# Optimization experiments

Measured on AMD Instinct MI355X. Metric: run time of the kernel, lower is better.

The kernel has to match this reference:

```python
import jax, jax.numpy as jnp
import numpy as np

VOCAB = 32
UTT_LEN = 16
NUM_MEANING_TYPES = 5
MEANINGS_PER_TYPE = 10
SUPPORT_SIZE = 100000  # = MEANINGS_PER_TYPE ** NUM_MEANING_TYPES
BATCH = 2048


def setup_inputs() -> dict:
    key = jax.random.key(0)
    k1, k2, k3 = jax.random.split(key, 3)
    # query utterances: [utt_len, batch] token ids
    utts = jax.random.randint(k1, (UTT_LEN, BATCH), 0, VOCAB, dtype=jnp.int64)
    # support set is stored as one-hot encoded utterances [S, utt_len*vocab]
    support_tokens = jax.random.randint(k2, (SUPPORT_SIZE, UTT_LEN), 0, VOCAB)
    support = jax.nn.one_hot(support_tokens, VOCAB, dtype=jnp.float32)
    support = support.reshape(SUPPORT_SIZE, UTT_LEN * VOCAB)
    # meanings table [S, num_meaning_types]
    meanings_t = jax.random.randint(k3, (SUPPORT_SIZE, NUM_MEANING_TYPES), 0,
                                    MEANINGS_PER_TYPE, dtype=jnp.int64)
    return {"utts": utts, "support": support, "meanings_t": meanings_t}


def reference(utts, support, meanings_t):
    # utts: [M, N] ints; support: [S, M*V] floats; meanings_t: [S, T] ints
    M, N = utts.shape
    # one-hot encode queries: [N, M, V] -> [N, M*V]
    batch_fluffy = jax.nn.one_hot(utts.T, VOCAB, dtype=jnp.float32).reshape(N, M * VOCAB)
    batch_sq = jnp.sum(batch_fluffy * batch_fluffy, axis=1)        # [N]
    support_sq = jnp.sum(support * support, axis=1)                # [S]
    cross = batch_fluffy @ support.T                                # [N, S]
    squared_dist = batch_sq[:, None] + support_sq[None, :] - 2.0 * cross
    # top-1 smallest distance (K=1)
    top1 = jnp.argmin(squared_dist, axis=1)                         # [N]
    meanings = meanings_t[top1]                                     # [N, T]
    return jax.nn.one_hot(meanings, MEANINGS_PER_TYPE, dtype=jnp.float32)
```

## Files before the change

kernel.cpp:

```cpp
#include <hip/hip_runtime.h>
#include <stdint.h>

#define S_ROWS 100000
#define NQ     2048
#define M_POS  16
#define VOCABS 32
#define WPB    8
#define GROUPS 8
#define CHUNKS 125
#define RC     800
#define KITER  25
#define KPAD   264

__global__ __launch_bounds__(256) void knn_decode(const float* __restrict__ support,
                                                  uint8_t* __restrict__ tok,
                                                  uint32_t* __restrict__ best) {
    if (blockIdx.x < 8) best[blockIdx.x * 256 + threadIdx.x] = 0u;
    int wave = (blockIdx.x * 256 + threadIdx.x) >> 6;
    int lane = threadIdx.x & 63;
    if (wave >= S_ROWS) return;
    const float4* rowp = (const float4*)(support + (size_t)wave * 512) + lane * 2;
    float4 f0 = rowp[0];
    float4 f1 = rowp[1];
    float base = (float)((lane & 3) * 64);
    float v = f0.x * (base + 0.f)  + f0.y * (base + 8.f)  + f0.z * (base + 16.f) + f0.w * (base + 24.f)
            + f1.x * (base + 32.f) + f1.y * (base + 40.f) + f1.z * (base + 48.f) + f1.w * (base + 56.f);
    v += __shfl_xor(v, 1);
    v += __shfl_xor(v, 2);
    if ((lane & 3) == 0) {
        int p = lane >> 2;
        tok[(size_t)wave * 16 + p] = (uint8_t)(v + 0.5f);
    }
}

__device__ __forceinline__ void FA(uint32_t a, uint32_t b, uint32_t c,
                                   uint32_t& s, uint32_t& co) {
    uint32_t x = a ^ b;
    s  = x ^ c;
    co = (a & b) | (x & c);
}
__device__ __forceinline__ void HA(uint32_t a, uint32_t b, uint32_t& s, uint32_t& co) {
    s = a ^ b; co = a & b;
}

__device__ __forceinline__ void gather16(const uint32_t* __restrict__ tw, uint4 ta,
                                         uint32_t b[16]) {
    b[0]  = tw[ (ta.x        & 0xFFu) +  0*256];
    b[1]  = tw[((ta.x >> 8)  & 0xFFu) +  1*256];
    b[2]  = tw[((ta.x >> 16) & 0xFFu) +  2*256];
    b[3]  = tw[((ta.x >> 24)        ) +  3*256];
    b[4]  = tw[ (ta.y        & 0xFFu) +  4*256];
    b[5]  = tw[((ta.y >> 8)  & 0xFFu) +  5*256];
    b[6]  = tw[((ta.y >> 16) & 0xFFu) +  6*256];
    b[7]  = tw[((ta.y >> 24)        ) +  7*256];
    b[8]  = tw[ (ta.z        & 0xFFu) +  8*256];
    b[9]  = tw[((ta.z >> 8)  & 0xFFu) +  9*256];
    b[10] = tw[((ta.z >> 16) & 0xFFu) + 10*256];
    b[11] = tw[((ta.z >> 24)        ) + 11*256];
    b[12] = tw[ (ta.w        & 0xFFu) + 12*256];
    b[13] = tw[((ta.w >> 8)  & 0xFFu) + 13*256];
    b[14] = tw[((ta.w >> 16) & 0xFFu) + 14*256];
    b[15] = tw[((ta.w >> 24)        ) + 15*256];
}

__device__ __forceinline__ void score_row(const uint32_t b[16], int k,
        uint32_t& cp0, uint32_t& cp1, uint32_t& cp2, uint32_t& cp3, uint32_t& cp4,
        uint32_t& k0p, uint32_t& k1p, uint32_t& k2p, uint32_t& k3p, uint32_t& k4p) {
    uint32_t s10,s11,s12,s13,s14, c10,c11,c12,c13,c14;
    FA(b[0],b[1],b[2],   s10,c10);
    FA(b[3],b[4],b[5],   s11,c11);
    FA(b[6],b[7],b[8],   s12,c12);
    FA(b[9],b[10],b[11], s13,c13);
    FA(b[12],b[13],b[14],s14,c14);
    uint32_t s2a,c2a,s2b,c2b;
    FA(s10,s11,s12, s2a,c2a);
    FA(s13,s14,b[15], s2b,c2b);
    uint32_t n0,h0;  HA(s2a,s2b, n0,h0);
    uint32_t u,cu,vv,cv,x2,cx,n1,cy;
    FA(c10,c11,c12, u,cu);
    FA(c13,c14,c2a, vv,cv);
    FA(u,vv,c2b,    x2,cx);
    HA(x2,h0,       n1,cy);
    uint32_t y4,cz,n2,cw,n3,n4;
    FA(cu,cv,cx, y4,cz);
    HA(y4,cy,    n2,cw);
    HA(cz,cw,    n3,n4);

    uint32_t eq = ~(n4 ^ cp4);
    uint32_t gt = n4 & ~cp4;
    gt |= eq & (n3 & ~cp3);  eq &= ~(n3 ^ cp3);
    gt |= eq & (n2 & ~cp2);  eq &= ~(n2 ^ cp2);
    gt |= eq & (n1 & ~cp1);  eq &= ~(n1 ^ cp1);
    gt |= eq & (n0 & ~cp0);

    uint32_t ng = ~gt;
    cp0 = (gt & n0) | (ng & cp0);
    cp1 = (gt & n1) | (ng & cp1);
    cp2 = (gt & n2) | (ng & cp2);
    cp3 = (gt & n3) | (ng & cp3);
    cp4 = (gt & n4) | (ng & cp4);
    uint32_t kb0 = 0u - (uint32_t)( k       & 1);
    uint32_t kb1 = 0u - (uint32_t)((k >> 1) & 1);
    uint32_t kb2 = 0u - (uint32_t)((k >> 2) & 1);
    uint32_t kb3 = 0u - (uint32_t)((k >> 3) & 1);
    uint32_t kb4 = 0u - (uint32_t)((k >> 4) & 1);
    k0p = (k0p & ng) | (gt & kb0);
    k1p = (k1p & ng) | (gt & kb1);
    k2p = (k2p & ng) | (gt & kb2);
    k3p = (k3p & ng) | (gt & kb3);
    k4p = (k4p & ng) | (gt & kb4);
}

__global__ __launch_bounds__(256, 4)
__attribute__((amdgpu_waves_per_eu(4, 4)))
void knn_score(const int* __restrict__ utts,
               const uint8_t* __restrict__ tok,
               uint32_t* __restrict__ best) {
    __shared__ uint32_t smem[32 * KPAD];
    uint32_t* table = smem;
    uint32_t* keys  = smem;

    const int bid = blockIdx.x;
    const int g   = bid & 7;
    const int c   = bid >> 3;
    const int t   = threadIdx.x;

    #pragma unroll
    for (int i = 0; i < 16; ++i) table[t + 256 * i] = 0u;
    __syncthreads();

    {
        int q = g * 256 + t;
        int wb = t >> 5, j = t & 31;
        #pragma unroll
        for (int m = 0; m < M_POS; ++m) {
            int v = utts[m * NQ + q];
            atomicOr(&table[(m * VOCABS + v) * WPB + wb], 1u << j);
        }
    }
    __syncthreads();

    const int w   = t & 7;
    const int sub = t >> 3;
    const int r0  = c * RC;
    const uint32_t* tw = table + w;

    uint32_t cp0=0,cp1=0,cp2=0,cp3=0,cp4=0;
    uint32_t k0p=0,k1p=0,k2p=0,k3p=0,k4p=0;

    const uint4* tbase = (const uint4*)(tok + (size_t)(r0 + sub) * 16);

    uint4 tA = tbase[0];
    uint4 tB = tbase[32];
    #pragma unroll 1
    for (int j = 0; j < 12; ++j) {
        uint4 tAn, tBn;
        if (j < 11) {
            tAn = tbase[32 * (2 * j + 2)];
            tBn = tbase[32 * (2 * j + 3)];
        } else {
            tAn = tbase[32 * 24];
            tBn = tAn;
        }
        uint32_t b0[16], b1[16];
        gather16(tw, tA, b0);
        gather16(tw, tB, b1);
        score_row(b0, 2 * j,     cp0,cp1,cp2,cp3,cp4, k0p,k1p,k2p,k3p,k4p);
        score_row(b1, 2 * j + 1, cp0,cp1,cp2,cp3,cp4, k0p,k1p,k2p,k3p,k4p);
        tA = tAn; tB = tBn;
    }
    {
        uint32_t b0[16];
        gather16(tw, tA, b0);
        score_row(b0, 24, cp0,cp1,cp2,cp3,cp4, k0p,k1p,k2p,k3p,k4p);
    }

    __syncthreads();

    {
        uint32_t C = 0x1FFFFu - (uint32_t)(r0 + sub);
        #pragma unroll
        for (int j = 0; j < 32; ++j) {
            uint32_t cnt = ((cp0>>j)&1u) | (((cp1>>j)&1u)<<1) | (((cp2>>j)&1u)<<2)
                         | (((cp3>>j)&1u)<<3) | (((cp4>>j)&1u)<<4);
            uint32_t kk  = ((k0p>>j)&1u) | (((k1p>>j)&1u)<<1) | (((k2p>>j)&1u)<<2)
                         | (((k3p>>j)&1u)<<3) | (((k4p>>j)&1u)<<4);
            uint32_t key = (cnt << 17) + C - (kk << 5);
            keys[j * KPAD + t] = key;
        }
    }
    __syncthreads();

    {
        int w2 = t & 7, j2 = t >> 3;
        const uint32_t* kp = keys + j2 * KPAD + w2;
        uint32_t bestv = 0;
        #pragma unroll
        for (int i = 0; i < 32; ++i) {
            uint32_t v = kp[8 * i];
            bestv = bestv > v ? bestv : v;
        }
        atomicMax(&best[g * 256 + w2 * 32 + j2], bestv);
    }
}

__global__ __launch_bounds__(256) void knn_out(const uint32_t* __restrict__ best,
                                               const int* __restrict__ meanings,
                                               float* __restrict__ out) {
    int q = blockIdx.x * 256 + threadIdx.x;
    if (q >= NQ) return;
    uint32_t b = best[q];
    int idx = 0x1FFFF - (int)(b & 0x1FFFFu);
    float* o = out + (size_t)q * 50;
    #pragma unroll
    for (int tt = 0; tt < 5; ++tt) {
        int mv = meanings[(size_t)idx * 5 + tt];
        #pragma unroll
        for (int mm = 0; mm < 10; ++mm) o[tt * 10 + mm] = (mm == mv) ? 1.0f : 0.0f;
    }
}

extern "C" void kernel_launch(void* const* d_in, const int* in_sizes, int n_in,
                              void* d_out, int out_size, void* d_ws, size_t ws_size,
                              hipStream_t stream) {
    const int*   utts     = (const int*)d_in[0];
    const float* support  = (const float*)d_in[1];
    const int*   meanings = (const int*)d_in[2];
    float* out = (float*)d_out;

    uint8_t*  tok  = (uint8_t*)d_ws;
    uint32_t* best = (uint32_t*)((char*)d_ws + (size_t)S_ROWS * 16);

    knn_decode<<<(S_ROWS + 3) / 4, 256, 0, stream>>>(support, tok, best);
    knn_score<<<GROUPS * CHUNKS, 256, 0, stream>>>(utts, tok, best);
    knn_out<<<NQ / 256, 256, 0, stream>>>(best, meanings, out);
}
```

Baseline: 314.3 us.

## Widen query tile to 1024 per block and reduce support rows per thread

Each score block now covers 1024 queries (32 bitmask words per table entry) instead of 256, so every decoded support-row token load and the address computation behind each gather serve four times as many queries. Rows per thread-column drop to 8 with 50 rows each, which needs a sixth bit for the row index, and there are now 500 blocks of the 2×250 grid. The bitset table grows to 64KB of LDS with occupancy lowered to 2 waves per EU. Fewer waves may hide LDS gather latency less well, and the larger table may conflict more in LDS banks.

Measured after the change: 352.9 us. 12.3% more time.

```diff
diff --git a/kernel.cpp b/kernel.cpp
--- a/kernel.cpp
+++ b/kernel.cpp
@@ -5,11 +5,11 @@
 #define NQ     2048
 #define M_POS  16
 #define VOCABS 32
-#define WPB    8
-#define GROUPS 8
-#define CHUNKS 125
-#define RC     800
-#define KITER  25
+#define GROUPS 2
+#define CHUNKS 250
+#define RC     400
+#define SUBS   8
+#define NPAIR  25
 #define KPAD   264
 
 __global__ __launch_bounds__(256) void knn_decode(const float* __restrict__ support,
@@ -43,29 +43,30 @@
     s = a ^ b; co = a & b;
 }
 
-__device__ __forceinline__ void gather16(const uint32_t* __restrict__ tw, uint4 ta,
+__device__ __forceinline__ void gather16(const char* __restrict__ tb, uint4 ta,
                                          uint32_t b[16]) {
-    b[0]  = tw[ (ta.x        & 0xFFu) +  0*256];
-    b[1]  = tw[((ta.x >> 8)  & 0xFFu) +  1*256];
-    b[2]  = tw[((ta.x >> 16) & 0xFFu) +  2*256];
-    b[3]  = tw[((ta.x >> 24)        ) +  3*256];
-    b[4]  = tw[ (ta.y        & 0xFFu) +  4*256];
-    b[5]  = tw[((ta.y >> 8)  & 0xFFu) +  5*256];
-    b[6]  = tw[((ta.y >> 16) & 0xFFu) +  6*256];
-    b[7]  = tw[((ta.y >> 24)        ) +  7*256];
-    b[8]  = tw[ (ta.z        & 0xFFu) +  8*256];
-    b[9]  = tw[((ta.z >> 8)  & 0xFFu) +  9*256];
-    b[10] = tw[((ta.z >> 16) & 0xFFu) + 10*256];
-    b[11] = tw[((ta.z >> 24)        ) + 11*256];
-    b[12] = tw[ (ta.w        & 0xFFu) + 12*256];
-    b[13] = tw[((ta.w >> 8)  & 0xFFu) + 13*256];
-    b[14] = tw[((ta.w >> 16) & 0xFFu) + 14*256];
-    b[15] = tw[((ta.w >> 24)        ) + 15*256];
+    b[0]  = *(const uint32_t*)(tb + ( ta.x        & 0xFFu) * 16 +  0*4096);
+    b[1]  = *(const uint32_t*)(tb + ((ta.x >> 8)  & 0xFFu) * 16 +  1*4096);
+    b[2]  = *(const uint32_t*)(tb + ((ta.x >> 16) & 0xFFu) * 16 +  2*4096);
+    b[3]  = *(const uint32_t*)(tb + ((ta.x >> 24)        ) * 16 +  3*4096);
+    b[4]  = *(const uint32_t*)(tb + ( ta.y        & 0xFFu) * 16 +  4*4096);
+    b[5]  = *(const uint32_t*)(tb + ((ta.y >> 8)  & 0xFFu) * 16 +  5*4096);
+    b[6]  = *(const uint32_t*)(tb + ((ta.y >> 16) & 0xFFu) * 16 +  6*4096);
+    b[7]  = *(const uint32_t*)(tb + ((ta.y >> 24)        ) * 16 +  7*4096);
+    b[8]  = *(const uint32_t*)(tb + ( ta.z        & 0xFFu) * 16 +  8*4096);
+    b[9]  = *(const uint32_t*)(tb + ((ta.z >> 8)  & 0xFFu) * 16 +  9*4096);
+    b[10] = *(const uint32_t*)(tb + ((ta.z >> 16) & 0xFFu) * 16 + 10*4096);
+    b[11] = *(const uint32_t*)(tb + ((ta.z >> 24)        ) * 16 + 11*4096);
+    b[12] = *(const uint32_t*)(tb + ( ta.w        & 0xFFu) * 16 + 12*4096);
+    b[13] = *(const uint32_t*)(tb + ((ta.w >> 8)  & 0xFFu) * 16 + 13*4096);
+    b[14] = *(const uint32_t*)(tb + ((ta.w >> 16) & 0xFFu) * 16 + 14*4096);
+    b[15] = *(const uint32_t*)(tb + ((ta.w >> 24)        ) * 16 + 15*4096);
 }
 
 __device__ __forceinline__ void score_row(const uint32_t b[16], int k,
         uint32_t& cp0, uint32_t& cp1, uint32_t& cp2, uint32_t& cp3, uint32_t& cp4,
-        uint32_t& k0p, uint32_t& k1p, uint32_t& k2p, uint32_t& k3p, uint32_t& k4p) {
+        uint32_t& k0p, uint32_t& k1p, uint32_t& k2p, uint32_t& k3p, uint32_t& k4p,
+        uint32_t& k5p) {
     uint32_t s10,s11,s12,s13,s14, c10,c11,c12,c13,c14;
     FA(b[0],b[1],b[2],   s10,c10);
     FA(b[3],b[4],b[5],   s11,c11);
@@ -104,75 +105,72 @@
     uint32_t kb2 = 0u - (uint32_t)((k >> 2) & 1);
     uint32_t kb3 = 0u - (uint32_t)((k >> 3) & 1);
     uint32_t kb4 = 0u - (uint32_t)((k >> 4) & 1);
+    uint32_t kb5 = 0u - (uint32_t)((k >> 5) & 1);
     k0p = (k0p & ng) | (gt & kb0);
     k1p = (k1p & ng) | (gt & kb1);
     k2p = (k2p & ng) | (gt & kb2);
     k3p = (k3p & ng) | (gt & kb3);
     k4p = (k4p & ng) | (gt & kb4);
-}
-
-__global__ __launch_bounds__(256, 4)
-__attribute__((amdgpu_waves_per_eu(4, 4)))
+    k5p = (k5p & ng) | (gt & kb5);
+}
+
+__global__ __launch_bounds__(256)
+__attribute__((amdgpu_waves_per_eu(2, 2)))
 void knn_score(const int* __restrict__ utts,
                const uint8_t* __restrict__ tok,
                uint32_t* __restrict__ best) {
-    __shared__ uint32_t smem[32 * KPAD];
-    uint32_t* table = smem;
-    uint32_t* keys  = smem;
+    __shared__ uint32_t smem[16384];
 
     const int bid = blockIdx.x;
-    const int g   = bid & 7;
-    const int c   = bid >> 3;
+    const int g   = bid & 1;
+    const int c   = bid >> 1;
     const int t   = threadIdx.x;
 
     #pragma unroll
-    for (int i = 0; i < 16; ++i) table[t + 256 * i] = 0u;
+    for (int i = 0; i < 64; ++i) smem[t + 256 * i] = 0u;
     __syncthreads();
 
     {
-        int q = g * 256 + t;
-        int wb = t >> 5, j = t & 31;
+        int wb = t >> 3;
+        int jb = (t & 7) * 4;
         #pragma unroll
         for (int m = 0; m < M_POS; ++m) {
-            int v = utts[m * NQ + q];
-            atomicOr(&table[(m * VOCABS + v) * WPB + wb], 1u << j);
-        }
-    }
-    __syncthreads();
-
-    const int w   = t & 7;
-    const int sub = t >> 3;
+            int4 q4 = *((const int4*)(utts + m * NQ + g * 1024) + t);
+            atomicOr(&smem[m * 1024 + q4.x * 32 + wb], 1u << (jb + 0));
+            atomicOr(&smem[m * 1024 + q4.y * 32 + wb], 1u << (jb + 1));
+            atomicOr(&smem[m * 1024 + q4.z * 32 + wb], 1u << (jb + 2));
+            atomicOr(&smem[m * 1024 + q4.w * 32 + wb], 1u << (jb + 3));
+        }
+    }
+    __syncthreads();
+
+    const int w   = t & 31;
+    const int sub = t >> 5;
     const int r0  = c * RC;
-    const uint32_t* tw = table + w;
+    const char* tb = (const char*)smem + w * 4;
 
     uint32_t cp0=0,cp1=0,cp2=0,cp3=0,cp4=0;
-    uint32_t k0p=0,k1p=0,k2p=0,k3p=0,k4p=0;
-
-    const uint4* tbase = (const uint4*)(tok + (size_t)(r0 + sub) * 16);
+    uint32_t k0p=0,k1p=0,k2p=0,k3p=0,k4p=0,k5p=0;
+
+    const uint4* tbase = (const uint4*)tok + (r0 + sub);
 
     uint4 tA = tbase[0];
-    uint4 tB = tbase[32];
+    uint4 tB = tbase[8];
     #pragma unroll 1
-    for (int j = 0; j < 12; ++j) {
+    for (int j = 0; j < NPAIR; ++j) {
         uint4 tAn, tBn;
-        if (j < 11) {
-            tAn = tbase[32 * (2 * j + 2)];
-            tBn = tbase[32 * (2 * j + 3)];
+        if (j + 1 < NPAIR) {
+            tAn = tbase[8 * (2 * j + 2)];
+            tBn = tbase[8 * (2 * j + 3)];
         } else {
-            tAn = tbase[32 * 24];
-            tBn = tAn;
+            tAn = tA; tBn = tB;
         }
         uint32_t b0[16], b1[16];
-        gather16(tw, tA, b0);
-        gather16(tw, tB, b1);
-        score_row(b0, 2 * j,     cp0,cp1,cp2,cp3,cp4, k0p,k1p,k2p,k3p,k4p);
-        score_row(b1, 2 * j + 1, cp0,cp1,cp2,cp3,cp4, k0p,k1p,k2p,k3p,k4p);
+        gather16(tb, tA, b0);
+        gather16(tb, tB, b1);
+        score_row(b0, 2 * j,     cp0,cp1,cp2,cp3,cp4, k0p,k1p,k2p,k3p,k4p,k5p);
+        score_row(b1, 2 * j + 1, cp0,cp1,cp2,cp3,cp4, k0p,k1p,k2p,k3p,k4p,k5p);
         tA = tAn; tB = tBn;
-    }
-    {
-        uint32_t b0[16];
-        gather16(tw, tA, b0);
-        score_row(b0, 24, cp0,cp1,cp2,cp3,cp4, k0p,k1p,k2p,k3p,k4p);
     }
 
     __syncthreads();
@@ -184,23 +182,26 @@
             uint32_t cnt = ((cp0>>j)&1u) | (((cp1>>j)&1u)<<1) | (((cp2>>j)&1u)<<2)
                          | (((cp3>>j)&1u)<<3) | (((cp4>>j)&1u)<<4);
             uint32_t kk  = ((k0p>>j)&1u) | (((k1p>>j)&1u)<<1) | (((k2p>>j)&1u)<<2)
-                         | (((k3p>>j)&1u)<<3) | (((k4p>>j)&1u)<<4);
-            uint32_t key = (cnt << 17) + C - (kk << 5);
-            keys[j * KPAD + t] = key;
+                         | (((k3p>>j)&1u)<<3) | (((k4p>>j)&1u)<<4) | (((k5p>>j)&1u)<<5);
+            uint32_t key = (cnt << 17) + C - (kk << 3);
+            smem[j * KPAD + t] = key;
         }
     }
     __syncthreads();
 
     {
-        int w2 = t & 7, j2 = t >> 3;
-        const uint32_t* kp = keys + j2 * KPAD + w2;
-        uint32_t bestv = 0;
-        #pragma unroll
-        for (int i = 0; i < 32; ++i) {
-            uint32_t v = kp[8 * i];
-            bestv = bestv > v ? bestv : v;
-        }
-        atomicMax(&best[g * 256 + w2 * 32 + j2], bestv);
+        int w2 = t & 31, j2 = t >> 5;
+        #pragma unroll
+        for (int jj = 0; jj < 4; ++jj) {
+            int j = j2 + 8 * jj;
+            uint32_t bestv = 0;
+            #pragma unroll
+            for (int s = 0; s < 8; ++s) {
+                uint32_t v = smem[j * KPAD + s * 32 + w2];
+                bestv = bestv > v ? bestv : v;
+            }
+            atomicMax(&best[g * 1024 + w2 * 32 + j], bestv);
+        }
     }
 }
 
```
